# Kernel optimization log

Measured on AMD Instinct MI355X. Metric: run time of the kernel, lower is better.

Reference implementation:

```python
import jax, jax.numpy as jnp
import numpy as np

B, T, DIM = 256, 2048, 64
THETA, MU, SIGMA = 0.1, 0.0, 1.0


def setup_inputs() -> dict:
    key = jax.random.key(0)
    k1, k2 = jax.random.split(key)
    # strictly increasing positive times, shape [B, T, 1]
    dt = jax.random.uniform(k1, (B, T, 1), minval=1e-3, maxval=1e-2, dtype=jnp.float32)
    ts = jnp.cumsum(dt, axis=1)
    # standard normal reparameterization noise for Normal(0, delta_ts).rsample()
    noise = jax.random.normal(k2, (B, T, DIM), dtype=jnp.float32)
    return {"ts": ts, "noise": noise}


def reference(ts, noise):
    h = DIM // 2  # slice_index
    # t_prev: 0 at step 0, ts[:, :-1] afterwards
    t_prev = jnp.concatenate([jnp.zeros_like(ts[:, :1]), ts[:, :-1]], axis=1)  # [B,T,1]
    # Brownian-increment std: sqrt(t_k - t_{k-1})  (sqrt(t_0) at k=0)
    db = jnp.sqrt(ts - t_prev)  # [B,T,1]
    # OU-increment std: sqrt(exp(2*theta*t_k) - exp(2*theta*t_{k-1}))  (exp(0)=1 at k=0)
    dou = jnp.sqrt(jnp.exp(2.0 * THETA * ts) - jnp.exp(2.0 * THETA * t_prev))  # [B,T,1]
    bt = ts.shape[:-1]
    delta = jnp.concatenate([jnp.broadcast_to(db, bt + (h,)),
                             jnp.broadcast_to(dou, bt + (h,))], axis=-1)  # [B,T,DIM]
    invalid = delta <= 0.0
    delta = jnp.where(invalid, delta + 1e-4, delta)
    # rsample = 0 + delta * eps; zero out invalid entries
    r = jnp.where(invalid, 0.0, delta * noise)
    # per-half scaling
    scale = jnp.concatenate([jnp.full((h,), np.sqrt(SIGMA), dtype=r.dtype),
                             jnp.full((h,), SIGMA / np.sqrt(2.0 * THETA), dtype=r.dtype)])
    r = r * scale
    out = jnp.cumsum(r, axis=-2)  # scan along time
    # OU mean-reversion transform on second half
    e = jnp.exp(-THETA * ts)  # [B,T,1]
    ou = e * out[..., h:] + MU * (1.0 - e)
    # normalize=True branch
    bm = out[..., :h] / (SIGMA * jnp.sqrt(ts) + 1e-8)
    ou = ou / (SIGMA * jnp.sqrt((1.0 - jnp.exp(-2.0 * THETA * ts)) / (2.0 * THETA)) + 1e-8)
    return jnp.concatenate([bm, ou], axis=-1)  # [B,T,DIM]
```

## Files before the change

kernel.cpp:

```cpp
#include <hip/hip_runtime.h>
#include <cstddef>

#define B_   256
#define T_   2048
#define DIM_ 64
#define NW   16
#define CH   (T_ / NW)
#define OU_SCALE 2.2360679774997896f

__global__ __launch_bounds__(1024) void fused_kernel(
        const float* __restrict__ ts,
        const float* __restrict__ noise,
        float* __restrict__ out)
{
    __shared__ float4 cofs[T_];
    __shared__ float4 par4[NW * 16];

    const int b   = blockIdx.x;
    const int tid = threadIdx.x;
    const int w   = tid >> 6;
    const int l   = tid & 63;

    const float* tsb = ts + (size_t)b * T_;
    for (int t = tid; t < T_; t += 1024) {
        float tk = tsb[t];
        float tp = (t == 0) ? 0.0f : tsb[t - 1];
        float dt = tk - tp;

        float db  = sqrtf(dt);
        float dou = sqrtf(expf(0.2f * tp) * expm1f(0.2f * dt));

        float cb = (db  <= 0.0f) ? 0.0f : db;
        float co = (dou <= 0.0f) ? 0.0f : dou * OU_SCALE;

        float fb = 1.0f / (sqrtf(tk) + 1e-8f);
        float em = expf(-0.1f * tk);
        float fo = em / (sqrtf(-expm1f(-0.2f * tk) * 5.0f) + 1e-8f);

        cofs[t] = make_float4(cb, co, fb, fo);
    }
    __syncthreads();

    const size_t rowbase = (size_t)b * T_ * DIM_;

    if (w != NW - 1) {
        const int  g   = l >> 4;
        const int  dq  = (l & 15) << 2;
        const bool ouA = (dq >= DIM_ / 2);
        const int  tb  = w * CH;
        float4 a = make_float4(0.f, 0.f, 0.f, 0.f);
#pragma unroll 8
        for (int i = 0; i < CH / 4; ++i) {
            const int t = tb + (i << 2) + g;
            const float4 v = *(const float4*)(noise + rowbase + (size_t)t * DIM_ + dq);
            const float4 c = cofs[t];
            const float delta = ouA ? c.y : c.x;
            a.x = fmaf(delta, v.x, a.x);
            a.y = fmaf(delta, v.y, a.y);
            a.z = fmaf(delta, v.z, a.z);
            a.w = fmaf(delta, v.w, a.w);
        }
        a.x += __shfl_xor(a.x, 16); a.y += __shfl_xor(a.y, 16);
        a.z += __shfl_xor(a.z, 16); a.w += __shfl_xor(a.w, 16);
        a.x += __shfl_xor(a.x, 32); a.y += __shfl_xor(a.y, 32);
        a.z += __shfl_xor(a.z, 32); a.w += __shfl_xor(a.w, 32);
        if (l < 16) par4[w * 16 + l] = a;
    }
    __syncthreads();

    const float* parf = (const float*)par4;
    float acc = 0.0f;
    for (int k = 0; k < w; ++k) acc += parf[k * DIM_ + l];

    const bool ou  = (l >= DIM_ / 2);
    const float* np_ = noise + rowbase + l;
    float*       op  = out   + rowbase + l;
    const int tb = w * CH;
#pragma unroll 8
    for (int t = tb; t < tb + CH; ++t) {
        float v = np_[(size_t)t * DIM_];
        float4 c = cofs[t];
        float delta = ou ? c.y : c.x;
        float f     = ou ? c.w : c.z;
        acc = fmaf(delta, v, acc);
        op[(size_t)t * DIM_] = acc * f;
    }
}

extern "C" void kernel_launch(void* const* d_in, const int* in_sizes, int n_in,
                              void* d_out, int out_size, void* d_ws, size_t ws_size,
                              hipStream_t stream) {
    const float* ts    = (const float*)d_in[0];
    const float* noise = (const float*)d_in[1];
    float* out = (float*)d_out;
    (void)d_ws; (void)ws_size;

    fused_kernel<<<B_, NW * 64, 0, stream>>>(ts, noise, out);
}
```

Before: 252.5 us.

## Split fused scan into two-pass chunked reduce-then-scan kernels with vectorized I/O

```diff
diff --git a/kernel.cpp b/kernel.cpp
--- a/kernel.cpp
+++ b/kernel.cpp
@@ -4,86 +4,146 @@
 #define B_   256
 #define T_   2048
 #define DIM_ 64
-#define NW   16
-#define CH   (T_ / NW)
+#define NC_  16
+#define CS_  (T_ / NC_)
+#define SG_  16
+#define SPS_ (CS_ / SG_)
 #define OU_SCALE 2.2360679774997896f
 
-__global__ __launch_bounds__(1024) void fused_kernel(
+__device__ __forceinline__ float2 delta_pair(const float* __restrict__ tsb, int t) {
+    float tk = tsb[t];
+    float tp = (t == 0) ? 0.0f : tsb[t - 1];
+    float dt = tk - tp;
+    float db  = sqrtf(dt);
+    float dou = sqrtf(expf(0.2f * tp) * expm1f(0.2f * dt));
+    float cb = (db  <= 0.0f) ? 0.0f : db;
+    float co = (dou <= 0.0f) ? 0.0f : dou * OU_SCALE;
+    return make_float2(cb, co);
+}
+
+__global__ __launch_bounds__(256) void partial_kernel(
         const float* __restrict__ ts,
         const float* __restrict__ noise,
+        float* __restrict__ partials)
+{
+    __shared__ float2 dlt[CS_];
+    __shared__ float4 red[SG_][16];
+
+    const int v   = blockIdx.x;
+    const int b   = v >> 4;
+    const int c   = v & (NC_ - 1);
+    const int tid = threadIdx.x;
+    const int sg  = tid >> 4;
+    const int qi  = tid & 15;
+    const int q   = qi << 2;
+    const int t0  = c * CS_;
+
+    const size_t rowbase = (size_t)b * T_ * DIM_;
+    const float* np = noise + rowbase + (size_t)(t0 + sg * SPS_) * DIM_ + q;
+    float4 r[SPS_];
+#pragma unroll
+    for (int i = 0; i < SPS_; ++i)
+        r[i] = *(const float4*)(np + (size_t)i * DIM_);
+
+    const float* tsb = ts + (size_t)b * T_;
+    if (tid < CS_) dlt[tid] = delta_pair(tsb, t0 + tid);
+    __syncthreads();
+
+    const bool ou = q >= (DIM_ / 2);
+    float4 a = make_float4(0.f, 0.f, 0.f, 0.f);
+#pragma unroll
+    for (int i = 0; i < SPS_; ++i) {
+        float2 d2 = dlt[sg * SPS_ + i];
+        float d = ou ? d2.y : d2.x;
+        a.x = fmaf(d, r[i].x, a.x);
+        a.y = fmaf(d, r[i].y, a.y);
+        a.z = fmaf(d, r[i].z, a.z);
+        a.w = fmaf(d, r[i].w, a.w);
+    }
+    red[sg][qi] = a;
+    __syncthreads();
+
+    if (tid < 16) {
+        float4 s = red[0][tid];
+#pragma unroll
+        for (int k = 1; k < SG_; ++k) {
+            float4 t4 = red[k][tid];
+            s.x += t4.x; s.y += t4.y; s.z += t4.z; s.w += t4.w;
+        }
+        *(float4*)(partials + ((size_t)b * NC_ + c) * DIM_ + (tid << 2)) = s;
+    }
+}
+
+__global__ __launch_bounds__(256) void scan_kernel(
+        const float* __restrict__ ts,
+        const float* __restrict__ noise,
+        const float* __restrict__ partials,
         float* __restrict__ out)
 {
-    __shared__ float4 cofs[T_];
-    __shared__ float4 par4[NW * 16];
+    __shared__ float4 cof[CS_];
+    __shared__ float4 red[SG_][16];
 
-    const int b   = blockIdx.x;
+    const int v   = blockIdx.x;
+    const int b   = v >> 4;
+    const int c   = v & (NC_ - 1);
     const int tid = threadIdx.x;
-    const int w   = tid >> 6;
-    const int l   = tid & 63;
+    const int sg  = tid >> 4;
+    const int qi  = tid & 15;
+    const int q   = qi << 2;
+    const int t0  = c * CS_;
+
+    const size_t rowbase = (size_t)b * T_ * DIM_;
+    const float* np = noise + rowbase + (size_t)(t0 + sg * SPS_) * DIM_ + q;
+    float4 r[SPS_];
+#pragma unroll
+    for (int i = 0; i < SPS_; ++i)
+        r[i] = *(const float4*)(np + (size_t)i * DIM_);
+
+    float4 base = make_float4(0.f, 0.f, 0.f, 0.f);
+    const float* pb = partials + (size_t)b * NC_ * DIM_ + q;
+    for (int k = 0; k < c; ++k) {
+        float4 p = *(const float4*)(pb + k * DIM_);
+        base.x += p.x; base.y += p.y; base.z += p.z; base.w += p.w;
+    }
 
     const float* tsb = ts + (size_t)b * T_;
-    for (int t = tid; t < T_; t += 1024) {
-        float tk = tsb[t];
-        float tp = (t == 0) ? 0.0f : tsb[t - 1];
-        float dt = tk - tp;
-
-        float db  = sqrtf(dt);
-        float dou = sqrtf(expf(0.2f * tp) * expm1f(0.2f * dt));
-
-        float cb = (db  <= 0.0f) ? 0.0f : db;
-        float co = (dou <= 0.0f) ? 0.0f : dou * OU_SCALE;
-
-        float fb = 1.0f / (sqrtf(tk) + 1e-8f);
-        float em = expf(-0.1f * tk);
-        float fo = em / (sqrtf(-expm1f(-0.2f * tk) * 5.0f) + 1e-8f);
-
-        cofs[t] = make_float4(cb, co, fb, fo);
+    if (tid < CS_) {
+        int t = t0 + tid;
+        float2 d  = delta_pair(tsb, t);
+        float tk  = tsb[t];
+        float fb  = 1.0f / (sqrtf(tk) + 1e-8f);
+        float em  = expf(-0.1f * tk);
+        float fo  = em / (sqrtf(-expm1f(-0.2f * tk) * 5.0f) + 1e-8f);
+        cof[t - t0] = make_float4(d.x, d.y, fb, fo);
     }
     __syncthreads();
 
-    const size_t rowbase = (size_t)b * T_ * DIM_;
-
-    if (w != NW - 1) {
-        const int  g   = l >> 4;
-        const int  dq  = (l & 15) << 2;
-        const bool ouA = (dq >= DIM_ / 2);
-        const int  tb  = w * CH;
-        float4 a = make_float4(0.f, 0.f, 0.f, 0.f);
-#pragma unroll 8
-        for (int i = 0; i < CH / 4; ++i) {
-            const int t = tb + (i << 2) + g;
-            const float4 v = *(const float4*)(noise + rowbase + (size_t)t * DIM_ + dq);
-            const float4 c = cofs[t];
-            const float delta = ouA ? c.y : c.x;
-            a.x = fmaf(delta, v.x, a.x);
-            a.y = fmaf(delta, v.y, a.y);
-            a.z = fmaf(delta, v.z, a.z);
-            a.w = fmaf(delta, v.w, a.w);
-        }
-        a.x += __shfl_xor(a.x, 16); a.y += __shfl_xor(a.y, 16);
-        a.z += __shfl_xor(a.z, 16); a.w += __shfl_xor(a.w, 16);
-        a.x += __shfl_xor(a.x, 32); a.y += __shfl_xor(a.y, 32);
-        a.z += __shfl_xor(a.z, 32); a.w += __shfl_xor(a.w, 32);
-        if (l < 16) par4[w * 16 + l] = a;
+    const bool ou = q >= (DIM_ / 2);
+    float4 s = make_float4(0.f, 0.f, 0.f, 0.f);
+#pragma unroll
+    for (int i = 0; i < SPS_; ++i) {
+        float4 cc = cof[sg * SPS_ + i];
+        float d = ou ? cc.y : cc.x;
+        r[i].x *= d; r[i].y *= d; r[i].z *= d; r[i].w *= d;
+        s.x += r[i].x; s.y += r[i].y; s.z += r[i].z; s.w += r[i].w;
     }
+    red[sg][qi] = s;
     __syncthreads();
 
-    const float* parf = (const float*)par4;
-    float acc = 0.0f;
-    for (int k = 0; k < w; ++k) acc += parf[k * DIM_ + l];
+    float4 acc = base;
+    for (int k = 0; k < sg; ++k) {
+        float4 p = red[k][qi];
+        acc.x += p.x; acc.y += p.y; acc.z += p.z; acc.w += p.w;
+    }
 
-    const bool ou  = (l >= DIM_ / 2);
-    const float* np_ = noise + rowbase + l;
-    float*       op  = out   + rowbase + l;
-    const int tb = w * CH;
-#pragma unroll 8
-    for (int t = tb; t < tb + CH; ++t) {
-        float v = np_[(size_t)t * DIM_];
-        float4 c = cofs[t];
-        float delta = ou ? c.y : c.x;
-        float f     = ou ? c.w : c.z;
-        acc = fmaf(delta, v, acc);
-        op[(size_t)t * DIM_] = acc * f;
+    float* op = out + rowbase + (size_t)(t0 + sg * SPS_) * DIM_ + q;
+#pragma unroll
+    for (int i = 0; i < SPS_; ++i) {
+        float4 cc = cof[sg * SPS_ + i];
+        float f = ou ? cc.w : cc.z;
+        acc.x += r[i].x; acc.y += r[i].y; acc.z += r[i].z; acc.w += r[i].w;
+        float4 o = make_float4(acc.x * f, acc.y * f, acc.z * f, acc.w * f);
+        *(float4*)(op + (size_t)i * DIM_) = o;
     }
 }
 
@@ -93,7 +153,9 @@
     const float* ts    = (const float*)d_in[0];
     const float* noise = (const float*)d_in[1];
     float* out = (float*)d_out;
-    (void)d_ws; (void)ws_size;
+    float* partials = (float*)d_ws;
+    (void)ws_size; (void)in_sizes; (void)n_in; (void)out_size;
 
-    fused_kernel<<<B_, NW * 64, 0, stream>>>(ts, noise, out);
+    partial_kernel<<<B_ * NC_, 256, 0, stream>>>(ts, noise, partials);
+    scan_kernel   <<<B_ * NC_, 256, 0, stream>>>(ts, noise, partials, out);
 }
```

New measurement: 265.7 us. 1.05x slower.

## Split time scan into 64 float4 segments per block with vectorized second pass

Applied to the files above, without the earlier changes.

```diff
diff --git a/kernel.cpp b/kernel.cpp
--- a/kernel.cpp
+++ b/kernel.cpp
@@ -4,8 +4,8 @@
 #define B_   256
 #define T_   2048
 #define DIM_ 64
-#define NW   16
-#define CH   (T_ / NW)
+#define SGN_ 64
+#define SPT_ (T_ / SGN_)
 #define OU_SCALE 2.2360679774997896f
 
 __global__ __launch_bounds__(1024) void fused_kernel(
@@ -14,76 +14,70 @@
         float* __restrict__ out)
 {
     __shared__ float4 cofs[T_];
-    __shared__ float4 par4[NW * 16];
+    __shared__ float4 par[SGN_][16];
 
     const int b   = blockIdx.x;
     const int tid = threadIdx.x;
-    const int w   = tid >> 6;
-    const int l   = tid & 63;
+    const int sg  = tid >> 4;
+    const int qi  = tid & 15;
+    const int q   = qi << 2;
 
     const float* tsb = ts + (size_t)b * T_;
     for (int t = tid; t < T_; t += 1024) {
-        float tk = tsb[t];
-        float tp = (t == 0) ? 0.0f : tsb[t - 1];
-        float dt = tk - tp;
-
-        float db  = sqrtf(dt);
-        float dou = sqrtf(expf(0.2f * tp) * expm1f(0.2f * dt));
-
-        float cb = (db  <= 0.0f) ? 0.0f : db;
-        float co = (dou <= 0.0f) ? 0.0f : dou * OU_SCALE;
-
-        float fb = 1.0f / (sqrtf(tk) + 1e-8f);
-        float em = expf(-0.1f * tk);
-        float fo = em / (sqrtf(-expm1f(-0.2f * tk) * 5.0f) + 1e-8f);
-
+        const float tk = tsb[t];
+        const float tp = (t == 0) ? 0.0f : tsb[t - 1];
+        const float dt = tk - tp;
+        const float db  = sqrtf(dt);
+        const float dou = sqrtf(expf(0.2f * tp) * expm1f(0.2f * dt));
+        const float cb = (db  <= 0.0f) ? 0.0f : db;
+        const float co = (dou <= 0.0f) ? 0.0f : dou * OU_SCALE;
+        const float fb = 1.0f / (sqrtf(tk) + 1e-8f);
+        const float em = expf(-0.1f * tk);
+        const float fo = em / (sqrtf(-expm1f(-0.2f * tk) * 5.0f) + 1e-8f);
         cofs[t] = make_float4(cb, co, fb, fo);
     }
     __syncthreads();
 
     const size_t rowbase = (size_t)b * T_ * DIM_;
+    const bool   ou      = q >= (DIM_ / 2);
+    const int    tb      = sg * SPT_;
+    const float* np = noise + rowbase + (size_t)tb * DIM_ + q;
 
-    if (w != NW - 1) {
-        const int  g   = l >> 4;
-        const int  dq  = (l & 15) << 2;
-        const bool ouA = (dq >= DIM_ / 2);
-        const int  tb  = w * CH;
+    {
         float4 a = make_float4(0.f, 0.f, 0.f, 0.f);
 #pragma unroll 8
-        for (int i = 0; i < CH / 4; ++i) {
-            const int t = tb + (i << 2) + g;
-            const float4 v = *(const float4*)(noise + rowbase + (size_t)t * DIM_ + dq);
-            const float4 c = cofs[t];
-            const float delta = ouA ? c.y : c.x;
-            a.x = fmaf(delta, v.x, a.x);
-            a.y = fmaf(delta, v.y, a.y);
-            a.z = fmaf(delta, v.z, a.z);
-            a.w = fmaf(delta, v.w, a.w);
+        for (int i = 0; i < SPT_; ++i) {
+            const float4 v = *(const float4*)(np + (size_t)i * DIM_);
+            const float4 c = cofs[tb + i];
+            const float  d = ou ? c.y : c.x;
+            a.x = fmaf(d, v.x, a.x);
+            a.y = fmaf(d, v.y, a.y);
+            a.z = fmaf(d, v.z, a.z);
+            a.w = fmaf(d, v.w, a.w);
         }
-        a.x += __shfl_xor(a.x, 16); a.y += __shfl_xor(a.y, 16);
-        a.z += __shfl_xor(a.z, 16); a.w += __shfl_xor(a.w, 16);
-        a.x += __shfl_xor(a.x, 32); a.y += __shfl_xor(a.y, 32);
-        a.z += __shfl_xor(a.z, 32); a.w += __shfl_xor(a.w, 32);
-        if (l < 16) par4[w * 16 + l] = a;
+        par[sg][qi] = a;
     }
     __syncthreads();
 
-    const float* parf = (const float*)par4;
-    float acc = 0.0f;
-    for (int k = 0; k < w; ++k) acc += parf[k * DIM_ + l];
+    float4 acc = make_float4(0.f, 0.f, 0.f, 0.f);
+    for (int k = 0; k < sg; ++k) {
+        const float4 p = par[k][qi];
+        acc.x += p.x; acc.y += p.y; acc.z += p.z; acc.w += p.w;
+    }
 
-    const bool ou  = (l >= DIM_ / 2);
-    const float* np_ = noise + rowbase + l;
-    float*       op  = out   + rowbase + l;
-    const int tb = w * CH;
+    float* op = out + rowbase + (size_t)tb * DIM_ + q;
 #pragma unroll 8
-    for (int t = tb; t < tb + CH; ++t) {
-        float v = np_[(size_t)t * DIM_];
-        float4 c = cofs[t];
-        float delta = ou ? c.y : c.x;
-        float f     = ou ? c.w : c.z;
-        acc = fmaf(delta, v, acc);
-        op[(size_t)t * DIM_] = acc * f;
+    for (int i = 0; i < SPT_; ++i) {
+        const float4 v = *(const float4*)(np + (size_t)i * DIM_);
+        const float4 c = cofs[tb + i];
+        const float  d = ou ? c.y : c.x;
+        const float  f = ou ? c.w : c.z;
+        acc.x = fmaf(d, v.x, acc.x);
+        acc.y = fmaf(d, v.y, acc.y);
+        acc.z = fmaf(d, v.z, acc.z);
+        acc.w = fmaf(d, v.w, acc.w);
+        *(float4*)(op + (size_t)i * DIM_) =
+            make_float4(acc.x * f, acc.y * f, acc.z * f, acc.w * f);
     }
 }
 
@@ -93,7 +87,7 @@
     const float* ts    = (const float*)d_in[0];
     const float* noise = (const float*)d_in[1];
     float* out = (float*)d_out;
-    (void)d_ws; (void)ws_size;
+    (void)d_ws; (void)ws_size; (void)in_sizes; (void)n_in; (void)out_size;
 
-    fused_kernel<<<B_, NW * 64, 0, stream>>>(ts, noise, out);
+    fused_kernel<<<B_, 1024, 0, stream>>>(ts, noise, out);
 }
```

After: 258.5 us. +2.4%, slower.
